# Kernel tuning notes

Hardware: AMD Instinct MI355X
Metric: run time of the kernel (lower is better)

The kernel has to match this reference:

```python
import jax, jax.numpy as jnp
from jax import lax
import numpy as np

T = 140
H = 64
B = 8192

def _uniform(key, shape, k):
    return jax.random.uniform(key, shape, dtype=jnp.float32, minval=-k, maxval=k)

def setup_inputs() -> dict:
    key = jax.random.key(0)
    ks = jax.random.split(key, 12)
    k = 1.0 / np.sqrt(H)  # torch default init bound
    return {
        "x": jax.random.normal(ks[0], (B, T, 1), dtype=jnp.float32),
        "h_state": jnp.zeros((2, B, H), dtype=jnp.float32),
        "W_ih0": _uniform(ks[1], (H, 1), k),
        "W_hh0": _uniform(ks[2], (H, H), k),
        "b_ih0": _uniform(ks[3], (H,), k),
        "b_hh0": _uniform(ks[4], (H,), k),
        "W_ih1": _uniform(ks[5], (H, H), k),
        "W_hh1": _uniform(ks[6], (H, H), k),
        "b_ih1": _uniform(ks[7], (H,), k),
        "b_hh1": _uniform(ks[8], (H,), k),
        "W_out": _uniform(ks[9], (1, H), k),
        "b_out": _uniform(ks[10], (1,), k),
    }

def reference(x, h_state, W_ih0, W_hh0, b_ih0, b_hh0, W_ih1, W_hh1, b_ih1, b_hh1, W_out, b_out):
    b = x.shape[0]
    x = x.reshape(b, T, 1)
    xs = jnp.swapaxes(x, 0, 1)  # [T, B, 1]

    def step(carry, xt):
        h0, h1 = carry
        # torch RNN cell: h_t = tanh(x W_ih^T + b_ih + h_{t-1} W_hh^T + b_hh)
        h0n = jnp.tanh(xt @ W_ih0.T + b_ih0 + h0 @ W_hh0.T + b_hh0)
        h1n = jnp.tanh(h0n @ W_ih1.T + b_ih1 + h1 @ W_hh1.T + b_hh1)
        return (h0n, h1n), h1n

    (hf0, hf1), ys = lax.scan(step, (h_state[0], h_state[1]), xs)
    ys = jnp.swapaxes(ys, 0, 1)  # [B, T, H]
    out = (ys @ W_out.T + b_out).reshape(b, T, 1)
    h_final = jnp.stack([hf0, hf1])  # [2, B, H]
    return out, h_final
```

## Files before the change

### kernel.cpp

```cpp
#include <hip/hip_runtime.h>

#define TT 140
#define BB 8192
#define HH 64
#define BT 16
#define HS 72
#define FP ((TT - 1) & 1)

typedef _Float16 half8 __attribute__((ext_vector_type(8)));
typedef _Float16 half4 __attribute__((ext_vector_type(4)));
typedef float    f32x4 __attribute__((ext_vector_type(4)));

#define MFMA16(a,b,c) __builtin_amdgcn_mfma_f32_16x16x32_f16(a, b, c, 0, 0, 0)

__device__ __forceinline__ float fast_tanh(float a) {
    float e = __builtin_amdgcn_exp2f(a * 2.88539008178f);
    return 1.0f - 2.0f * __builtin_amdgcn_rcpf(e + 1.0f);
}

__device__ __forceinline__ half8 ld_frag(const _Float16* p) {
    return *(const half8*)__builtin_assume_aligned(p, 16);
}

__device__ __forceinline__ half8 cvt_frag16(const float* p) {
    f32x4 wa = *(const f32x4*)p;
    f32x4 wb = *(const f32x4*)(p + 4);
    half8 h;
    #pragma unroll
    for (int j = 0; j < 8; ++j) h[j] = (_Float16)((j < 4) ? wa[j] : wb[j - 4]);
    return h;
}

__global__ __launch_bounds__(256, 2)
void rnn_kernel(const float* __restrict__ x,
                const float* __restrict__ h_state,
                const float* __restrict__ W_ih0,
                const float* __restrict__ W_hh0,
                const float* __restrict__ b_ih0,
                const float* __restrict__ b_hh0,
                const float* __restrict__ W_ih1,
                const float* __restrict__ W_hh1,
                const float* __restrict__ b_ih1,
                const float* __restrict__ b_hh1,
                const float* __restrict__ W_out,
                const float* __restrict__ b_out,
                float* __restrict__ out)
{
    __shared__ __align__(16) _Float16 h0f[2][BT * HS];
    __shared__ __align__(16) _Float16 h1f[2][BT * HS];
    __shared__ float xs[TT * 17];
    __shared__ float pps[TT * 68];

    const int tid  = threadIdx.x;
    const int w    = tid >> 6;
    const int lane = tid & 63;
    const int col  = lane & 15;
    const int q    = lane >> 4;
    const int b0   = blockIdx.x * BT;

    half8 A0[2], AI[2], AH[2];
    #pragma unroll
    for (int kt = 0; kt < 2; ++kt) {
        const int off = (16 * w + col) * HH + 32 * kt + 8 * q;
        A0[kt] = cvt_frag16(W_hh0 + off);
        AI[kt] = cvt_frag16(W_ih1 + off);
        AH[kt] = cvt_frag16(W_hh1 + off);
    }
    float e00[4], e10[4], e01[4], e11[4];
    #pragma unroll
    for (int r = 0; r < 4; ++r) {
        int j = 16 * w + 4 * q + r;
        e00[r] = b_ih0[j] + b_hh0[j];  e10[r] = W_ih0[j];
        e01[r] = b_ih1[j] + b_hh1[j];  e11[r] = W_out[j];
    }
    const float bout = b_out[0];

    for (int c = 0; c < (TT * BT + 255) / 256; ++c) {
        int i = c * 256 + tid;
        if (i < TT * BT) {
            int t = i >> 4, b = i & 15;
            xs[t * 17 + b] = x[(size_t)(b0 + b) * TT + t];
        }
    }
    #pragma unroll
    for (int c = 0; c < (BT * HH) / 256; ++c) {
        int i = c * 256 + tid;
        int b = i >> 6, u = i & 63;
        h0f[1][b * HS + u] = (_Float16)h_state[(size_t)(b0 + b) * HH + u];
        h1f[1][b * HS + u] = (_Float16)h_state[(size_t)BB * HH + (size_t)(b0 + b) * HH + u];
    }
    __syncthreads();

    for (int p = 0; p <= TT; ++p) {
        const int rb = (p + 1) & 1;
        const int wb = p & 1;
        half8 H0a = ld_frag(&h0f[rb][col * HS + 8 * q]);
        half8 H0b = ld_frag(&h0f[rb][col * HS + 32 + 8 * q]);
        half8 H1a = ld_frag(&h1f[wb][col * HS + 8 * q]);
        half8 H1b = ld_frag(&h1f[wb][col * HS + 32 + 8 * q]);
        float xt  = xs[p * 17 + col];

        if (p < TT) {
            f32x4 c = {0.f, 0.f, 0.f, 0.f};
            c = MFMA16(A0[0], H0a, c);
            c = MFMA16(A0[1], H0b, c);
            half4 h4;
            #pragma unroll
            for (int r = 0; r < 4; ++r) {
                float pre = c[r] + e00[r] + e10[r] * xt;
                h4[r] = (_Float16)fast_tanh(pre);
            }
            *(half4*)(&h0f[wb][col * HS + 16 * w + 4 * q]) = h4;
        }
        if (p >= 1) {
            f32x4 ci = {0.f, 0.f, 0.f, 0.f}, ch = {0.f, 0.f, 0.f, 0.f};
            ci = MFMA16(AI[0], H0a, ci);
            ci = MFMA16(AI[1], H0b, ci);
            ch = MFMA16(AH[0], H1a, ch);
            ch = MFMA16(AH[1], H1b, ch);
            f32x4 a = ci + ch;
            float pr = 0.f;
            half4 h4;
            #pragma unroll
            for (int r = 0; r < 4; ++r) {
                float pre = a[r] + e01[r];
                float hn  = fast_tanh(pre);
                pr += hn * e11[r];
                h4[r] = (_Float16)hn;
            }
            *(half4*)(&h1f[rb][col * HS + 16 * w + 4 * q]) = h4;
            pr += __shfl_xor(pr, 16, 64);
            pr += __shfl_xor(pr, 32, 64);
            if (lane < 16) pps[(p - 1) * 68 + w * 17 + lane] = pr;
        }
        __syncthreads();
    }

    #pragma unroll
    for (int bq = 0; bq < 4; ++bq) {
        int b = 4 * bq + w;
        #pragma unroll
        for (int c = 0; c < 3; ++c) {
            int t = c * 64 + lane;
            if (t < TT)
                out[(size_t)(b0 + b) * TT + t] =
                    pps[t * 68 + b] + pps[t * 68 + 17 + b]
                  + pps[t * 68 + 34 + b] + pps[t * 68 + 51 + b] + bout;
        }
    }
    const size_t OFF = (size_t)BB * TT;
    #pragma unroll
    for (int c = 0; c < (BT * HH) / 256; ++c) {
        int i = c * 256 + tid;
        int b = i >> 6, u = i & 63;
        out[OFF + (size_t)(b0 + b) * HH + u] = (float)h0f[FP][b * HS + u];
        out[OFF + (size_t)BB * HH + (size_t)(b0 + b) * HH + u] = (float)h1f[FP][b * HS + u];
    }
}

extern "C" void kernel_launch(void* const* d_in, const int* in_sizes, int n_in,
                              void* d_out, int out_size, void* d_ws, size_t ws_size,
                              hipStream_t stream) {
    const float* x      = (const float*)d_in[0];
    const float* hst    = (const float*)d_in[1];
    const float* W_ih0  = (const float*)d_in[2];
    const float* W_hh0  = (const float*)d_in[3];
    const float* b_ih0  = (const float*)d_in[4];
    const float* b_hh0  = (const float*)d_in[5];
    const float* W_ih1  = (const float*)d_in[6];
    const float* W_hh1  = (const float*)d_in[7];
    const float* b_ih1  = (const float*)d_in[8];
    const float* b_hh1  = (const float*)d_in[9];
    const float* W_out  = (const float*)d_in[10];
    const float* b_outp = (const float*)d_in[11];
    float* out = (float*)d_out;

    dim3 grid(BB / BT);
    dim3 block(256);
    rnn_kernel<<<grid, block, 0, stream>>>(x, hst, W_ih0, W_hh0, b_ih0, b_hh0,
                                           W_ih1, W_hh1, b_ih1, b_hh1,
                                           W_out, b_outp, out);
}
```

Before: 151.1 us.

## Fragment-major LDS hidden-state layout, prescaled tanh weights, bias folded into MFMA accumulator

Hidden states in LDS move from a padded row layout to a fragment-major [kt][slot][8] layout, so each lane's half8 MFMA operand read is contiguous and conflict-free. Weights and biases are prescaled by 2/ln2 when loaded, which removes the per-element multiply inside tanh. The bias and input terms now seed the MFMA accumulator instead of being added afterwards. s_setprio raises wave priority around the MFMA chains. Prescaling before the fp16 conversion slightly changes rounding of the weights.

```diff
diff --git a/kernel.cpp b/kernel.cpp
--- a/kernel.cpp
+++ b/kernel.cpp
@@ -4,8 +4,8 @@
 #define BB 8192
 #define HH 64
 #define BT 16
-#define HS 72
 #define FP ((TT - 1) & 1)
+#define K_TANH 2.88539008178f
 
 typedef _Float16 half8 __attribute__((ext_vector_type(8)));
 typedef _Float16 half4 __attribute__((ext_vector_type(4)));
@@ -13,8 +13,8 @@
 
 #define MFMA16(a,b,c) __builtin_amdgcn_mfma_f32_16x16x32_f16(a, b, c, 0, 0, 0)
 
-__device__ __forceinline__ float fast_tanh(float a) {
-    float e = __builtin_amdgcn_exp2f(a * 2.88539008178f);
+__device__ __forceinline__ float tanh_ps(float as) {
+    float e = __builtin_amdgcn_exp2f(as);
     return 1.0f - 2.0f * __builtin_amdgcn_rcpf(e + 1.0f);
 }
 
@@ -22,12 +22,13 @@
     return *(const half8*)__builtin_assume_aligned(p, 16);
 }
 
-__device__ __forceinline__ half8 cvt_frag16(const float* p) {
+__device__ __forceinline__ half8 cvt_frag16s(const float* p) {
     f32x4 wa = *(const f32x4*)p;
     f32x4 wb = *(const f32x4*)(p + 4);
     half8 h;
     #pragma unroll
-    for (int j = 0; j < 8; ++j) h[j] = (_Float16)((j < 4) ? wa[j] : wb[j - 4]);
+    for (int j = 0; j < 8; ++j)
+        h[j] = (_Float16)(K_TANH * ((j < 4) ? wa[j] : wb[j - 4]));
     return h;
 }
 
@@ -46,92 +47,99 @@
                 const float* __restrict__ b_out,
                 float* __restrict__ out)
 {
-    __shared__ __align__(16) _Float16 h0f[2][BT * HS];
-    __shared__ __align__(16) _Float16 h1f[2][BT * HS];
+    __shared__ __align__(16) _Float16 h0f[2][2][64][8];
+    __shared__ __align__(16) _Float16 h1f[2][2][64][8];
     __shared__ float xs[TT * 17];
     __shared__ float pps[TT * 68];
 
     const int tid  = threadIdx.x;
     const int w    = tid >> 6;
     const int lane = tid & 63;
-    const int col  = lane & 15;
+    const int n    = lane & 15;
     const int q    = lane >> 4;
     const int b0   = blockIdx.x * BT;
 
     half8 A0[2], AI[2], AH[2];
     #pragma unroll
     for (int kt = 0; kt < 2; ++kt) {
-        const int off = (16 * w + col) * HH + 32 * kt + 8 * q;
-        A0[kt] = cvt_frag16(W_hh0 + off);
-        AI[kt] = cvt_frag16(W_ih1 + off);
-        AH[kt] = cvt_frag16(W_hh1 + off);
+        const int off = (16 * w + n) * HH + 32 * kt + 8 * q;
+        A0[kt] = cvt_frag16s(W_hh0 + off);
+        AI[kt] = cvt_frag16s(W_ih1 + off);
+        AH[kt] = cvt_frag16s(W_hh1 + off);
     }
-    float e00[4], e10[4], e01[4], e11[4];
+    float e00[4], e10[4], e01[4], WO[4];
     #pragma unroll
     for (int r = 0; r < 4; ++r) {
         int j = 16 * w + 4 * q + r;
-        e00[r] = b_ih0[j] + b_hh0[j];  e10[r] = W_ih0[j];
-        e01[r] = b_ih1[j] + b_hh1[j];  e11[r] = W_out[j];
+        e00[r] = K_TANH * (b_ih0[j] + b_hh0[j]);
+        e10[r] = K_TANH * W_ih0[j];
+        e01[r] = K_TANH * (b_ih1[j] + b_hh1[j]);
+        WO[r]  = W_out[j];
     }
     const float bout = b_out[0];
 
-    for (int c = 0; c < (TT * BT + 255) / 256; ++c) {
-        int i = c * 256 + tid;
-        if (i < TT * BT) {
-            int t = i >> 4, b = i & 15;
-            xs[t * 17 + b] = x[(size_t)(b0 + b) * TT + t];
-        }
+    for (int i = tid; i < TT * BT; i += 256) {
+        int t = i >> 4, b = i & 15;
+        xs[t * 17 + b] = x[(size_t)(b0 + b) * TT + t];
     }
-    #pragma unroll
-    for (int c = 0; c < (BT * HH) / 256; ++c) {
-        int i = c * 256 + tid;
+    for (int i = tid; i < BT * HH; i += 256) {
         int b = i >> 6, u = i & 63;
-        h0f[1][b * HS + u] = (_Float16)h_state[(size_t)(b0 + b) * HH + u];
-        h1f[1][b * HS + u] = (_Float16)h_state[(size_t)BB * HH + (size_t)(b0 + b) * HH + u];
+        h0f[1][u >> 5][((u >> 3) & 3) * 16 + b][u & 7] =
+            (_Float16)h_state[(size_t)(b0 + b) * HH + u];
+        h1f[1][u >> 5][((u >> 3) & 3) * 16 + b][u & 7] =
+            (_Float16)h_state[(size_t)BB * HH + (size_t)(b0 + b) * HH + u];
     }
     __syncthreads();
+
+    const int rdslot = q * 16 + n;
+    const int u0  = 16 * w + 4 * q;
+    const int wkt = u0 >> 5, wqp = (u0 >> 3) & 3, woff = u0 & 7;
 
     for (int p = 0; p <= TT; ++p) {
         const int rb = (p + 1) & 1;
         const int wb = p & 1;
-        half8 H0a = ld_frag(&h0f[rb][col * HS + 8 * q]);
-        half8 H0b = ld_frag(&h0f[rb][col * HS + 32 + 8 * q]);
-        half8 H1a = ld_frag(&h1f[wb][col * HS + 8 * q]);
-        half8 H1b = ld_frag(&h1f[wb][col * HS + 32 + 8 * q]);
-        float xt  = xs[p * 17 + col];
+        half8 H0a = ld_frag(&h0f[rb][0][rdslot][0]);
+        half8 H0b = ld_frag(&h0f[rb][1][rdslot][0]);
+        half8 H1a = ld_frag(&h1f[wb][0][rdslot][0]);
+        half8 H1b = ld_frag(&h1f[wb][1][rdslot][0]);
+        float xt  = xs[p * 17 + n];
 
         if (p < TT) {
-            f32x4 c = {0.f, 0.f, 0.f, 0.f};
+            f32x4 c;
+            #pragma unroll
+            for (int r = 0; r < 4; ++r) c[r] = e00[r] + e10[r] * xt;
+            __builtin_amdgcn_s_setprio(1);
             c = MFMA16(A0[0], H0a, c);
             c = MFMA16(A0[1], H0b, c);
+            __builtin_amdgcn_s_setprio(0);
             half4 h4;
             #pragma unroll
-            for (int r = 0; r < 4; ++r) {
-                float pre = c[r] + e00[r] + e10[r] * xt;
-                h4[r] = (_Float16)fast_tanh(pre);
-            }
-            *(half4*)(&h0f[wb][col * HS + 16 * w + 4 * q]) = h4;
+            for (int r = 0; r < 4; ++r) h4[r] = (_Float16)tanh_ps(c[r]);
+            *(half4*)(&h0f[wb][wkt][wqp * 16 + n][woff]) = h4;
         }
         if (p >= 1) {
-            f32x4 ci = {0.f, 0.f, 0.f, 0.f}, ch = {0.f, 0.f, 0.f, 0.f};
+            f32x4 ci, ch = {0.f, 0.f, 0.f, 0.f};
+            #pragma unroll
+            for (int r = 0; r < 4; ++r) ci[r] = e01[r];
+            __builtin_amdgcn_s_setprio(1);
             ci = MFMA16(AI[0], H0a, ci);
             ci = MFMA16(AI[1], H0b, ci);
             ch = MFMA16(AH[0], H1a, ch);
             ch = MFMA16(AH[1], H1b, ch);
+            __builtin_amdgcn_s_setprio(0);
             f32x4 a = ci + ch;
             float pr = 0.f;
             half4 h4;
             #pragma unroll
             for (int r = 0; r < 4; ++r) {
-                float pre = a[r] + e01[r];
-                float hn  = fast_tanh(pre);
-                pr += hn * e11[r];
+                float hn = tanh_ps(a[r]);
+                pr += hn * WO[r];
                 h4[r] = (_Float16)hn;
             }
-            *(half4*)(&h1f[rb][col * HS + 16 * w + 4 * q]) = h4;
+            *(half4*)(&h1f[rb][wkt][wqp * 16 + n][woff]) = h4;
             pr += __shfl_xor(pr, 16, 64);
             pr += __shfl_xor(pr, 32, 64);
-            if (lane < 16) pps[(p - 1) * 68 + w * 17 + lane] = pr;
+            if (lane < 16) pps[(p - 1) * 68 + w * 17 + n] = pr;
         }
         __syncthreads();
     }
@@ -149,12 +157,12 @@
         }
     }
     const size_t OFF = (size_t)BB * TT;
-    #pragma unroll
-    for (int c = 0; c < (BT * HH) / 256; ++c) {
-        int i = c * 256 + tid;
+    for (int i = tid; i < BT * HH; i += 256) {
         int b = i >> 6, u = i & 63;
-        out[OFF + (size_t)(b0 + b) * HH + u] = (float)h0f[FP][b * HS + u];
-        out[OFF + (size_t)BB * HH + (size_t)(b0 + b) * HH + u] = (float)h1f[FP][b * HS + u];
+        out[OFF + (size_t)(b0 + b) * HH + u] =
+            (float)h0f[FP][u >> 5][((u >> 3) & 3) * 16 + b][u & 7];
+        out[OFF + (size_t)BB * HH + (size_t)(b0 + b) * HH + u] =
+            (float)h1f[FP][u >> 5][((u >> 3) & 3) * 16 + b][u & 7];
     }
 }
 
```

New measurement: 151.8 us. About the same (+0.5%).
